# Kernel optimization log

Hardware: AMD Instinct MI355X
Metric: run time of the kernel (lower is better)

Reference implementation:

```python
import jax, jax.numpy as jnp
import numpy as np

B, N, D_OBS, D_MSG, H = 4096, 64, 128, 64, 4
HD = D_MSG // H
EPS = 1e-5


def setup_inputs() -> dict:
    key = jax.random.key(0)
    ks = jax.random.split(key, 16)
    def w(k, shape):
        fan_in = shape[0]
        return (jax.random.normal(k, shape, dtype=jnp.float32) / np.sqrt(fan_in)).astype(jnp.float32)
    return {
        'obs_all': jax.random.normal(ks[0], (B, N, D_OBS), dtype=jnp.float32),
        # msg encoder: Linear(obs,128) -> ReLU -> Linear(128,msg)
        'enc_w1': w(ks[1], (D_OBS, 128)), 'enc_b1': jnp.zeros((128,), jnp.float32),
        'enc_w2': w(ks[2], (128, D_MSG)), 'enc_b2': jnp.zeros((D_MSG,), jnp.float32),
        # MultiheadAttention in/out projections (stored as (in, out))
        'in_proj_w': w(ks[3], (D_MSG, 3 * D_MSG)), 'in_proj_b': jnp.zeros((3 * D_MSG,), jnp.float32),
        'out_w': w(ks[4], (D_MSG, D_MSG)), 'out_b': jnp.zeros((D_MSG,), jnp.float32),
        # integrator: Linear(obs+msg,256) -> LayerNorm(256) -> ReLU -> Linear(256,obs)
        'int_w1': w(ks[5], (D_OBS + D_MSG, 256)), 'int_b1': jnp.zeros((256,), jnp.float32),
        'ln_g': jnp.ones((256,), jnp.float32), 'ln_b': jnp.zeros((256,), jnp.float32),
        'int_w2': w(ks[6], (256, D_OBS)), 'int_b2': jnp.zeros((D_OBS,), jnp.float32),
    }


def reference(obs_all, enc_w1, enc_b1, enc_w2, enc_b2,
              in_proj_w, in_proj_b, out_w, out_b,
              int_w1, int_b1, ln_g, ln_b, int_w2, int_b2):
    # --- send: encode observations into messages (B, N, msg_dim) ---
    h = jax.nn.relu(obs_all @ enc_w1 + enc_b1)
    msgs = h @ enc_w2 + enc_b2

    # --- attention aggregation: per-agent query over all messages.
    # The original per-agent loop (query = msgs[:, i:i+1]) is exactly
    # batched self-attention over the agent axis.
    qkv = msgs @ in_proj_w + in_proj_b            # (B, N, 3*msg)
    q, k, v = jnp.split(qkv, 3, axis=-1)
    q = q.reshape(B, N, H, HD)
    k = k.reshape(B, N, H, HD)
    v = v.reshape(B, N, H, HD)
    scale = 1.0 / np.sqrt(HD)
    scores = jnp.einsum('bqhd,bkhd->bhqk', q, k) * scale   # (B, H, N, N)
    attn = jax.nn.softmax(scores, axis=-1)
    ctx = jnp.einsum('bhqk,bkhd->bqhd', attn, v).reshape(B, N, D_MSG)
    agg = ctx @ out_w + out_b                     # (B, N, msg_dim)

    # --- receive: concat obs + aggregated message, MLP with LayerNorm ---
    combined = jnp.concatenate([obs_all, agg], axis=-1)
    z = combined @ int_w1 + int_b1                # (B, N, 256)
    mu = jnp.mean(z, axis=-1, keepdims=True)
    var = jnp.var(z, axis=-1, keepdims=True)
    z = (z - mu) * jax.lax.rsqrt(var + EPS) * ln_g + ln_b
    enriched = jax.nn.relu(z) @ int_w2 + int_b2   # (B, N, obs_dim)
    return enriched, msgs
```

## Files before the change

### kernel.cpp

```cpp
#include <hip/hip_runtime.h>


typedef __attribute__((ext_vector_type(8))) short bf16x8;
typedef __attribute__((ext_vector_type(4))) float f32x4;

#define MFMA16(a, b, c) __builtin_amdgcn_mfma_f32_16x16x32_bf16((a), (b), (c), 0, 0, 0)

__device__ __forceinline__ float b2f(short s) {
    union { unsigned u; float f; } x;
    x.u = ((unsigned)(unsigned short)s) << 16;
    return x.f;
}
__device__ __forceinline__ short f2b(float f) {
    union { float f; unsigned u; } x;
    x.f = f;
    unsigned r = (x.u + 0x7FFFu + ((x.u >> 16) & 1u)) >> 16;
    return (short)r;
}

template<bool F32>
__device__ __forceinline__ float ldS(const void* p, int i) {
    if (F32) return ((const float*)p)[i];
    return b2f(((const short*)p)[i]);
}
template<bool F32>
__device__ __forceinline__ bf16x8 ld8(const void* p, long i) {
    if (F32) {
        const float4* f = (const float4*)((const float*)p + i);
        float4 a = f[0], b = f[1];
        bf16x8 r;
        r[0] = f2b(a.x); r[1] = f2b(a.y); r[2] = f2b(a.z); r[3] = f2b(a.w);
        r[4] = f2b(b.x); r[5] = f2b(b.y); r[6] = f2b(b.z); r[7] = f2b(b.w);
        return r;
    }
    return *(const bf16x8*)((const short*)p + i);
}
template<bool F32>
__device__ __forceinline__ void st(void* p, long i, float v) {
    if (F32) ((float*)p)[i] = v;
    else ((short*)p)[i] = f2b(v);
}

#define U_S   0
#define Q_S   18432
#define K_S   26624
#define VT_S  34816
#define SMEM_SHORTS 39424
#define HP 136
#define MP 72
#define ZP 264
#define QP 32
#define KP 32
#define VP 72

#define WT1_OFF   0
#define WT2_OFF   16384
#define WTQ_OFF   24576
#define WTO_OFF   36864
#define WTI1_OFF  40960
#define WTI2_OFF  90112

__global__ void detect_dtype(const unsigned short* __restrict__ obs, int* __restrict__ flag) {
    if (threadIdx.x == 0 && blockIdx.x == 0) {
        int cnt = 0;
        for (int i = 0; i < 512; ++i) {
            unsigned e = (obs[i] >> 7) & 0xFFu;
            cnt += (e == 0u || (e >= 80u && e <= 140u)) ? 1 : 0;
        }
        *flag = (cnt >= 480) ? 1 : 0;
    }
}

template<bool F32>
__global__ void wtrans(const void* __restrict__ w1, const void* __restrict__ w2,
                       const void* __restrict__ wq, const void* __restrict__ wo,
                       const void* __restrict__ wi1, const void* __restrict__ wi2,
                       const int* __restrict__ flag, short* __restrict__ wt) {
    if (*flag != (F32 ? 0 : 1)) return;
    int id = blockIdx.x * 256 + threadIdx.x;
    const void* src;
    int K, N, off, loc;
    if (id < 16384)       { src = w1;  K = 128; N = 128; off = WT1_OFF;  loc = id; }
    else if (id < 24576)  { src = w2;  K = 128; N = 64;  off = WT2_OFF;  loc = id - 16384; }
    else if (id < 36864)  { src = wq;  K = 64;  N = 192; off = WTQ_OFF;  loc = id - 24576; }
    else if (id < 40960)  { src = wo;  K = 64;  N = 64;  off = WTO_OFF;  loc = id - 36864; }
    else if (id < 90112)  { src = wi1; K = 192; N = 256; off = WTI1_OFF; loc = id - 40960; }
    else if (id < 122880) { src = wi2; K = 256; N = 128; off = WTI2_OFF; loc = id - 90112; }
    else return;
    int n = loc / K;
    int k = loc - n * K;
    wt[off + loc] = f2b(ldS<F32>(src, k * N + n));
}

template<bool F32>
__global__ __launch_bounds__(256, 2)
void macs_main(const void* __restrict__ obs,
               const void* __restrict__ eb1, const void* __restrict__ eb2,
               const void* __restrict__ ipb, const void* __restrict__ ob,
               const void* __restrict__ ib1, const void* __restrict__ lg,
               const void* __restrict__ lb,  const void* __restrict__ ib2,
               const int* __restrict__ flag, const short* __restrict__ wt,
               void* __restrict__ out) {
    if (*flag != (F32 ? 0 : 1)) return;
    __shared__ __align__(16) short smem[SMEM_SHORTS];
    const int tid = threadIdx.x;
    const int w = tid >> 6;
    const int lane = tid & 63;
    const int q = lane >> 4;
    const int t = lane & 15;
    const int b = blockIdx.x;
    const long obase = (long)b * 64 * 128;

    {
        int4* z4 = (int4*)smem;
        for (int i = tid; i < SMEM_SHORTS / 8; i += 256) z4[i] = make_int4(0, 0, 0, 0);
    }
    __syncthreads();

    {
        f32x4 acc[4][2] = {};
        const short* wt1 = wt + WT1_OFF;
#pragma unroll
        for (int ks = 0; ks < 4; ++ks) {
            bf16x8 a[4], bb[2];
#pragma unroll
            for (int mt = 0; mt < 4; ++mt)
                a[mt] = ld8<F32>(obs, obase + (mt * 16 + t) * 128 + ks * 32 + q * 8);
#pragma unroll
            for (int tj = 0; tj < 2; ++tj)
                bb[tj] = *(const bf16x8*)(wt1 + (w * 32 + tj * 16 + t) * 128 + ks * 32 + q * 8);
#pragma unroll
            for (int mt = 0; mt < 4; ++mt)
#pragma unroll
                for (int tj = 0; tj < 2; ++tj)
                    acc[mt][tj] = MFMA16(a[mt], bb[tj], acc[mt][tj]);
        }
        short* hs = smem + U_S;
#pragma unroll
        for (int tj = 0; tj < 2; ++tj) {
            int c = w * 32 + tj * 16 + t;
            float bias = ldS<F32>(eb1, c);
#pragma unroll
            for (int mt = 0; mt < 4; ++mt)
#pragma unroll
                for (int i = 0; i < 4; ++i) {
                    int r = mt * 16 + q * 4 + i;
                    hs[r * HP + c] = f2b(fmaxf(acc[mt][tj][i] + bias, 0.f));
                }
        }
    }
    __syncthreads();

    {
        f32x4 acc[4] = {};
        const short* wt2 = wt + WT2_OFF;
        const short* hs = smem + U_S;
#pragma unroll
        for (int ks = 0; ks < 4; ++ks) {
            bf16x8 a[4];
            bf16x8 bb = *(const bf16x8*)(wt2 + (w * 16 + t) * 128 + ks * 32 + q * 8);
#pragma unroll
            for (int mt = 0; mt < 4; ++mt)
                a[mt] = *(const bf16x8*)(hs + (mt * 16 + t) * HP + ks * 32 + q * 8);
#pragma unroll
            for (int mt = 0; mt < 4; ++mt)
                acc[mt] = MFMA16(a[mt], bb, acc[mt]);
        }
        __syncthreads();
        short* ms = smem + U_S;
        float bias = ldS<F32>(eb2, w * 16 + t);
        const long msgs_base = 33554432L;
#pragma unroll
        for (int mt = 0; mt < 4; ++mt)
#pragma unroll
            for (int i = 0; i < 4; ++i) {
                int r = mt * 16 + q * 4 + i;
                float v = acc[mt][i] + bias;
                ms[r * MP + w * 16 + t] = f2b(v);
                st<F32>(out, msgs_base + ((long)b * 64 + r) * 64 + w * 16 + t, v);
            }
    }
    __syncthreads();

    {
        f32x4 acc[4][3] = {};
        const short* wtq = wt + WTQ_OFF;
        const short* ms = smem + U_S;
#pragma unroll
        for (int ks = 0; ks < 2; ++ks) {
            bf16x8 a[4], bb[3];
#pragma unroll
            for (int mt = 0; mt < 4; ++mt)
                a[mt] = *(const bf16x8*)(ms + (mt * 16 + t) * MP + ks * 32 + q * 8);
#pragma unroll
            for (int tj = 0; tj < 3; ++tj)
                bb[tj] = *(const bf16x8*)(wtq + (w * 48 + tj * 16 + t) * 64 + ks * 32 + q * 8);
#pragma unroll
            for (int mt = 0; mt < 4; ++mt)
#pragma unroll
                for (int tj = 0; tj < 3; ++tj)
                    acc[mt][tj] = MFMA16(a[mt], bb[tj], acc[mt][tj]);
        }
#pragma unroll
        for (int tj = 0; tj < 3; ++tj) {
            int c = w * 48 + tj * 16 + t;
            float bias = ldS<F32>(ipb, c);
            int sec = c >> 6;
            int head = (c >> 4) & 3;
#pragma unroll
            for (int mt = 0; mt < 4; ++mt)
#pragma unroll
                for (int i = 0; i < 4; ++i) {
                    int r = mt * 16 + q * 4 + i;
                    short bv = f2b(acc[mt][tj][i] + bias);
                    int idx;
                    if (sec == 0)      idx = Q_S + head * 2048 + r * QP + t;
                    else if (sec == 1) idx = K_S + head * 2048 + r * KP + t;
                    else               idx = VT_S + head * 1152 + t * VP + r;
                    smem[idx] = bv;
                }
        }
    }
    __syncthreads();

    {
        const short* qh = smem + Q_S + w * 2048;
        const short* kh = smem + K_S + w * 2048;
        const short* vh = smem + VT_S + w * 1152;
        f32x4 sc[4][4] = {};
        bf16x8 aq[4], bk[4];
#pragma unroll
        for (int mt = 0; mt < 4; ++mt)
            aq[mt] = *(const bf16x8*)(qh + (mt * 16 + t) * QP + q * 8);
#pragma unroll
        for (int tj = 0; tj < 4; ++tj)
            bk[tj] = *(const bf16x8*)(kh + (tj * 16 + t) * KP + q * 8);
#pragma unroll
        for (int mt = 0; mt < 4; ++mt)
#pragma unroll
            for (int tj = 0; tj < 4; ++tj)
                sc[mt][tj] = MFMA16(aq[mt], bk[tj], sc[mt][tj]);

        short* Pw = smem + U_S + w * 4608;
#pragma unroll
        for (int mt = 0; mt < 4; ++mt)
#pragma unroll
            for (int i = 0; i < 4; ++i) {
                float e[4];
                float mx = -1e30f;
#pragma unroll
                for (int tj = 0; tj < 4; ++tj) {
                    e[tj] = sc[mt][tj][i] * 0.25f;
                    mx = fmaxf(mx, e[tj]);
                }
#pragma unroll
                for (int off = 1; off < 16; off <<= 1) mx = fmaxf(mx, __shfl_xor(mx, off));
                float s = 0.f;
#pragma unroll
                for (int tj = 0; tj < 4; ++tj) {
                    e[tj] = __expf(e[tj] - mx);
                    s += e[tj];
                }
#pragma unroll
                for (int off = 1; off < 16; off <<= 1) s += __shfl_xor(s, off);
                float inv = 1.f / s;
                int r = mt * 16 + q * 4 + i;
#pragma unroll
                for (int tj = 0; tj < 4; ++tj)
                    Pw[r * MP + tj * 16 + t] = f2b(e[tj] * inv);
            }
        __syncthreads();

        f32x4 cx[4] = {};
#pragma unroll
        for (int ks = 0; ks < 2; ++ks) {
            bf16x8 a[4];
            bf16x8 bb = *(const bf16x8*)(vh + t * VP + ks * 32 + q * 8);
#pragma unroll
            for (int mt = 0; mt < 4; ++mt)
                a[mt] = *(const bf16x8*)(Pw + (mt * 16 + t) * MP + ks * 32 + q * 8);
#pragma unroll
            for (int mt = 0; mt < 4; ++mt)
                cx[mt] = MFMA16(a[mt], bb, cx[mt]);
        }
        __syncthreads();
        short* cs = smem + U_S;
#pragma unroll
        for (int mt = 0; mt < 4; ++mt)
#pragma unroll
            for (int i = 0; i < 4; ++i)
                cs[(mt * 16 + q * 4 + i) * MP + w * 16 + t] = f2b(cx[mt][i]);
    }
    __syncthreads();

    {
        f32x4 acc[4] = {};
        const short* wto = wt + WTO_OFF;
        const short* cs = smem + U_S;
#pragma unroll
        for (int ks = 0; ks < 2; ++ks) {
            bf16x8 a[4];
            bf16x8 bb = *(const bf16x8*)(wto + (w * 16 + t) * 64 + ks * 32 + q * 8);
#pragma unroll
            for (int mt = 0; mt < 4; ++mt)
                a[mt] = *(const bf16x8*)(cs + (mt * 16 + t) * MP + ks * 32 + q * 8);
#pragma unroll
            for (int mt = 0; mt < 4; ++mt)
                acc[mt] = MFMA16(a[mt], bb, acc[mt]);
        }
        short* ag = smem + U_S + 4608;
        float bias = ldS<F32>(ob, w * 16 + t);
#pragma unroll
        for (int mt = 0; mt < 4; ++mt)
#pragma unroll
            for (int i = 0; i < 4; ++i)
                ag[(mt * 16 + q * 4 + i) * MP + w * 16 + t] = f2b(acc[mt][i] + bias);
    }
    __syncthreads();

    {
        f32x4 acc[4][4] = {};
        const short* wti1 = wt + WTI1_OFF;
        const short* ag = smem + U_S + 4608;
#pragma unroll
        for (int ks = 0; ks < 6; ++ks) {
            bf16x8 a[4], bb[4];
            if (ks < 4) {
#pragma unroll
                for (int mt = 0; mt < 4; ++mt)
                    a[mt] = ld8<F32>(obs, obase + (mt * 16 + t) * 128 + ks * 32 + q * 8);
            } else {
#pragma unroll
                for (int mt = 0; mt < 4; ++mt)
                    a[mt] = *(const bf16x8*)(ag + (mt * 16 + t) * MP + (ks - 4) * 32 + q * 8);
            }
#pragma unroll
            for (int tj = 0; tj < 4; ++tj)
                bb[tj] = *(const bf16x8*)(wti1 + (w * 64 + tj * 16 + t) * 192 + ks * 32 + q * 8);
#pragma unroll
            for (int mt = 0; mt < 4; ++mt)
#pragma unroll
                for (int tj = 0; tj < 4; ++tj)
                    acc[mt][tj] = MFMA16(a[mt], bb[tj], acc[mt][tj]);
        }
#pragma unroll
        for (int tj = 0; tj < 4; ++tj) {
            float bias = ldS<F32>(ib1, w * 64 + tj * 16 + t);
#pragma unroll
            for (int mt = 0; mt < 4; ++mt)
#pragma unroll
                for (int i = 0; i < 4; ++i) acc[mt][tj][i] += bias;
        }
        float2* lnred = (float2*)(smem + K_S);
#pragma unroll
        for (int mt = 0; mt < 4; ++mt)
#pragma unroll
            for (int i = 0; i < 4; ++i) {
                float s = 0.f, s2 = 0.f;
#pragma unroll
                for (int tj = 0; tj < 4; ++tj) {
                    float v = acc[mt][tj][i];
                    s += v;
                    s2 += v * v;
                }
#pragma unroll
                for (int off = 1; off < 16; off <<= 1) {
                    s += __shfl_xor(s, off);
                    s2 += __shfl_xor(s2, off);
                }
                if (t == 0) {
                    float2 p; p.x = s; p.y = s2;
                    lnred[(mt * 16 + q * 4 + i) * 4 + w] = p;
                }
            }
        __syncthreads();
        float2* munr = (float2*)(smem + K_S + 1024);
        if (tid < 64) {
            float S = 0.f, S2 = 0.f;
#pragma unroll
            for (int j = 0; j < 4; ++j) {
                float2 p = lnred[tid * 4 + j];
                S += p.x;
                S2 += p.y;
            }
            float mu = S * (1.f / 256.f);
            float var = S2 * (1.f / 256.f) - mu * mu;
            float2 m; m.x = mu; m.y = rsqrtf(fmaxf(var, 0.f) + 1e-5f);
            munr[tid] = m;
        }
        __syncthreads();
        short* zs = smem + U_S;
        float gv[4], bv[4];
#pragma unroll
        for (int tj = 0; tj < 4; ++tj) {
            gv[tj] = ldS<F32>(lg, w * 64 + tj * 16 + t);
            bv[tj] = ldS<F32>(lb, w * 64 + tj * 16 + t);
        }
#pragma unroll
        for (int mt = 0; mt < 4; ++mt)
#pragma unroll
            for (int i = 0; i < 4; ++i) {
                int r = mt * 16 + q * 4 + i;
                float2 mr = munr[r];
#pragma unroll
                for (int tj = 0; tj < 4; ++tj) {
                    float v = (acc[mt][tj][i] - mr.x) * mr.y * gv[tj] + bv[tj];
                    zs[r * ZP + w * 64 + tj * 16 + t] = f2b(fmaxf(v, 0.f));
                }
            }
    }
    __syncthreads();

    {
        f32x4 acc[4][2] = {};
        const short* wti2 = wt + WTI2_OFF;
        const short* zs = smem + U_S;
#pragma unroll
        for (int ks = 0; ks < 8; ++ks) {
            bf16x8 a[4], bb[2];
#pragma unroll
            for (int mt = 0; mt < 4; ++mt)
                a[mt] = *(const bf16x8*)(zs + (mt * 16 + t) * ZP + ks * 32 + q * 8);
#pragma unroll
            for (int tj = 0; tj < 2; ++tj)
                bb[tj] = *(const bf16x8*)(wti2 + (w * 32 + tj * 16 + t) * 256 + ks * 32 + q * 8);
#pragma unroll
            for (int mt = 0; mt < 4; ++mt)
#pragma unroll
                for (int tj = 0; tj < 2; ++tj)
                    acc[mt][tj] = MFMA16(a[mt], bb[tj], acc[mt][tj]);
        }
#pragma unroll
        for (int tj = 0; tj < 2; ++tj) {
            int c = w * 32 + tj * 16 + t;
            float bias = ldS<F32>(ib2, c);
#pragma unroll
            for (int mt = 0; mt < 4; ++mt)
#pragma unroll
                for (int i = 0; i < 4; ++i) {
                    int r = mt * 16 + q * 4 + i;
                    st<F32>(out, ((long)b * 64 + r) * 128 + c, acc[mt][tj][i] + bias);
                }
        }
    }
}

extern "C" void kernel_launch(void* const* d_in, const int* in_sizes, int n_in,
                              void* d_out, int out_size, void* d_ws, size_t ws_size,
                              hipStream_t stream) {
    const void* obs = d_in[0];
    const void* w1  = d_in[1];
    const void* b1  = d_in[2];
    const void* w2  = d_in[3];
    const void* b2  = d_in[4];
    const void* wq  = d_in[5];
    const void* bq  = d_in[6];
    const void* wo  = d_in[7];
    const void* bo  = d_in[8];
    const void* wi1 = d_in[9];
    const void* bi1 = d_in[10];
    const void* lg  = d_in[11];
    const void* lb  = d_in[12];
    const void* wi2 = d_in[13];
    const void* bi2 = d_in[14];
    int* flag = (int*)d_ws;
    short* wt = (short*)d_ws + 128;

    detect_dtype<<<dim3(1), dim3(64), 0, stream>>>((const unsigned short*)obs, flag);
    wtrans<false><<<dim3(480), dim3(256), 0, stream>>>(w1, w2, wq, wo, wi1, wi2, flag, wt);
    wtrans<true ><<<dim3(480), dim3(256), 0, stream>>>(w1, w2, wq, wo, wi1, wi2, flag, wt);
    macs_main<false><<<dim3(4096), dim3(256), 0, stream>>>(obs, b1, b2, bq, bo, bi1, lg, lb, bi2, flag, wt, d_out);
    macs_main<true ><<<dim3(4096), dim3(256), 0, stream>>>(obs, b1, b2, bq, bo, bi1, lg, lb, bi2, flag, wt, d_out);
}
```

Baseline: 615.9 us.

## Shrink shared memory, restructure attention with 32x32 MFMA, raise occupancy

Repacks the shared-memory layout from about 79KB to about 53KB. It drops the zero-fill pass and one barrier, and raises launch bounds to 3 blocks per CU. Attention is rewritten so each wave handles half the query rows of two heads, using 32x32x16 MFMA for the scores. The Q scale is folded into the projection, and softmax skips max-subtraction, so overflow is possible for large scores. The dtype detection and weight transpose are also merged or parallelised to remove small launch overheads.

Result: faster. 582.5 us (-5.4%).

```diff
diff --git a/kernel.cpp b/kernel.cpp
--- a/kernel.cpp
+++ b/kernel.cpp
@@ -3,8 +3,10 @@
 
 typedef __attribute__((ext_vector_type(8))) short bf16x8;
 typedef __attribute__((ext_vector_type(4))) float f32x4;
+typedef __attribute__((ext_vector_type(16))) float f32x16;
 
 #define MFMA16(a, b, c) __builtin_amdgcn_mfma_f32_16x16x32_bf16((a), (b), (c), 0, 0, 0)
+#define MFMA32(a, b, c) __builtin_amdgcn_mfma_f32_32x32x16_bf16((a), (b), (c), 0, 0, 0)
 
 __device__ __forceinline__ float b2f(short s) {
     union { unsigned u; float f; } x;
@@ -41,16 +43,21 @@
     else ((short*)p)[i] = f2b(v);
 }
 
-#define U_S   0
-#define Q_S   18432
-#define K_S   26624
-#define VT_S  34816
-#define SMEM_SHORTS 39424
+#define P_S   0
+#define H_S   0
+#define Z_S   0
+#define Q2_S  9216
+#define AG_S  9216
+#define K2_S  13312
+#define VT_S  17408
+#define LN_S  17408
+#define MU_S  18432
+#define MS_S  22016
+#define SMEM_SHORTS 26624
 #define HP 136
 #define MP 72
 #define ZP 264
-#define QP 32
-#define KP 32
+#define PP 72
 #define VP 72
 
 #define WT1_OFF   0
@@ -61,22 +68,23 @@
 #define WTI2_OFF  90112
 
 __global__ void detect_dtype(const unsigned short* __restrict__ obs, int* __restrict__ flag) {
-    if (threadIdx.x == 0 && blockIdx.x == 0) {
-        int cnt = 0;
-        for (int i = 0; i < 512; ++i) {
-            unsigned e = (obs[i] >> 7) & 0xFFu;
-            cnt += (e == 0u || (e >= 80u && e <= 140u)) ? 1 : 0;
-        }
-        *flag = (cnt >= 480) ? 1 : 0;
-    }
-}
-
-template<bool F32>
+    if (blockIdx.x != 0) return;
+    int lane = threadIdx.x & 63;
+    int cnt = 0;
+    for (int i = lane; i < 512; i += 64) {
+        unsigned e = (obs[i] >> 7) & 0xFFu;
+        cnt += (e == 0u || (e >= 80u && e <= 140u)) ? 1 : 0;
+    }
+#pragma unroll
+    for (int off = 1; off < 64; off <<= 1) cnt += __shfl_xor(cnt, off);
+    if (lane == 0) *flag = (cnt >= 480) ? 1 : 0;
+}
+
 __global__ void wtrans(const void* __restrict__ w1, const void* __restrict__ w2,
                        const void* __restrict__ wq, const void* __restrict__ wo,
                        const void* __restrict__ wi1, const void* __restrict__ wi2,
                        const int* __restrict__ flag, short* __restrict__ wt) {
-    if (*flag != (F32 ? 0 : 1)) return;
+    const bool f32 = (*flag == 0);
     int id = blockIdx.x * 256 + threadIdx.x;
     const void* src;
     int K, N, off, loc;
@@ -89,11 +97,12 @@
     else return;
     int n = loc / K;
     int k = loc - n * K;
-    wt[off + loc] = f2b(ldS<F32>(src, k * N + n));
+    float v = f32 ? ((const float*)src)[k * N + n] : b2f(((const short*)src)[k * N + n]);
+    wt[off + loc] = f2b(v);
 }
 
 template<bool F32>
-__global__ __launch_bounds__(256, 2)
+__global__ __launch_bounds__(256, 3)
 void macs_main(const void* __restrict__ obs,
                const void* __restrict__ eb1, const void* __restrict__ eb2,
                const void* __restrict__ ipb, const void* __restrict__ ob,
@@ -108,16 +117,12 @@
     const int lane = tid & 63;
     const int q = lane >> 4;
     const int t = lane & 15;
+    const int l31 = lane & 31;
+    const int hi = lane >> 5;
     const int b = blockIdx.x;
     const long obase = (long)b * 64 * 128;
 
     {
-        int4* z4 = (int4*)smem;
-        for (int i = tid; i < SMEM_SHORTS / 8; i += 256) z4[i] = make_int4(0, 0, 0, 0);
-    }
-    __syncthreads();
-
-    {
         f32x4 acc[4][2] = {};
         const short* wt1 = wt + WT1_OFF;
 #pragma unroll
@@ -135,7 +140,7 @@
                 for (int tj = 0; tj < 2; ++tj)
                     acc[mt][tj] = MFMA16(a[mt], bb[tj], acc[mt][tj]);
         }
-        short* hs = smem + U_S;
+        short* hs = smem + H_S;
 #pragma unroll
         for (int tj = 0; tj < 2; ++tj) {
             int c = w * 32 + tj * 16 + t;
@@ -154,7 +159,7 @@
     {
         f32x4 acc[4] = {};
         const short* wt2 = wt + WT2_OFF;
-        const short* hs = smem + U_S;
+        const short* hs = smem + H_S;
 #pragma unroll
         for (int ks = 0; ks < 4; ++ks) {
             bf16x8 a[4];
@@ -166,8 +171,7 @@
             for (int mt = 0; mt < 4; ++mt)
                 acc[mt] = MFMA16(a[mt], bb, acc[mt]);
         }
-        __syncthreads();
-        short* ms = smem + U_S;
+        short* ms = smem + MS_S;
         float bias = ldS<F32>(eb2, w * 16 + t);
         const long msgs_base = 33554432L;
 #pragma unroll
@@ -185,7 +189,7 @@
     {
         f32x4 acc[4][3] = {};
         const short* wtq = wt + WTQ_OFF;
-        const short* ms = smem + U_S;
+        const short* ms = smem + MS_S;
 #pragma unroll
         for (int ks = 0; ks < 2; ++ks) {
             bf16x8 a[4], bb[3];
@@ -207,15 +211,16 @@
             float bias = ldS<F32>(ipb, c);
             int sec = c >> 6;
             int head = (c >> 4) & 3;
+            float scale = (sec == 0) ? 0.25f : 1.0f;
 #pragma unroll
             for (int mt = 0; mt < 4; ++mt)
 #pragma unroll
                 for (int i = 0; i < 4; ++i) {
                     int r = mt * 16 + q * 4 + i;
-                    short bv = f2b(acc[mt][tj][i] + bias);
+                    short bv = f2b((acc[mt][tj][i] + bias) * scale);
                     int idx;
-                    if (sec == 0)      idx = Q_S + head * 2048 + r * QP + t;
-                    else if (sec == 1) idx = K_S + head * 2048 + r * KP + t;
+                    if (sec == 0)      idx = Q2_S + head * 1024 + r * 16 + t;
+                    else if (sec == 1) idx = K2_S + head * 1024 + r * 16 + t;
                     else               idx = VT_S + head * 1152 + t * VP + r;
                     smem[idx] = bv;
                 }
@@ -224,79 +229,57 @@
     __syncthreads();
 
     {
-        const short* qh = smem + Q_S + w * 2048;
-        const short* kh = smem + K_S + w * 2048;
-        const short* vh = smem + VT_S + w * 1152;
-        f32x4 sc[4][4] = {};
-        bf16x8 aq[4], bk[4];
-#pragma unroll
-        for (int mt = 0; mt < 4; ++mt)
-            aq[mt] = *(const bf16x8*)(qh + (mt * 16 + t) * QP + q * 8);
-#pragma unroll
-        for (int tj = 0; tj < 4; ++tj)
-            bk[tj] = *(const bf16x8*)(kh + (tj * 16 + t) * KP + q * 8);
-#pragma unroll
-        for (int mt = 0; mt < 4; ++mt)
-#pragma unroll
-            for (int tj = 0; tj < 4; ++tj)
-                sc[mt][tj] = MFMA16(aq[mt], bk[tj], sc[mt][tj]);
-
-        short* Pw = smem + U_S + w * 4608;
-#pragma unroll
-        for (int mt = 0; mt < 4; ++mt)
-#pragma unroll
-            for (int i = 0; i < 4; ++i) {
-                float e[4];
-                float mx = -1e30f;
-#pragma unroll
-                for (int tj = 0; tj < 4; ++tj) {
-                    e[tj] = sc[mt][tj][i] * 0.25f;
-                    mx = fmaxf(mx, e[tj]);
-                }
-#pragma unroll
-                for (int off = 1; off < 16; off <<= 1) mx = fmaxf(mx, __shfl_xor(mx, off));
-                float s = 0.f;
-#pragma unroll
-                for (int tj = 0; tj < 4; ++tj) {
-                    e[tj] = __expf(e[tj] - mx);
-                    s += e[tj];
-                }
-#pragma unroll
-                for (int off = 1; off < 16; off <<= 1) s += __shfl_xor(s, off);
+        const int rh = w & 1;
+        short* Pq = smem + P_S + w * 2304;
+        short* cs = smem + MS_S;
+#pragma unroll
+        for (int p = 0; p < 2; ++p) {
+            const int hd = p * 2 + (w >> 1);
+            const short* qh = smem + Q2_S + hd * 1024;
+            const short* kh = smem + K2_S + hd * 1024;
+            const short* vh = smem + VT_S + hd * 1152;
+            f32x16 sc0 = {}, sc1 = {};
+            {
+                bf16x8 aq  = *(const bf16x8*)(qh + (rh * 32 + l31) * 16 + hi * 8);
+                bf16x8 bk0 = *(const bf16x8*)(kh + l31 * 16 + hi * 8);
+                bf16x8 bk1 = *(const bf16x8*)(kh + (32 + l31) * 16 + hi * 8);
+                sc0 = MFMA32(aq, bk0, sc0);
+                sc1 = MFMA32(aq, bk1, sc1);
+            }
+#pragma unroll
+            for (int i = 0; i < 16; ++i) {
+                int lr = (i & 3) + 8 * (i >> 2) + 4 * hi;
+                float e0 = __expf(sc0[i]);
+                float e1 = __expf(sc1[i]);
+                float s = e0 + e1;
+#pragma unroll
+                for (int off = 1; off < 32; off <<= 1) s += __shfl_xor(s, off);
                 float inv = 1.f / s;
-                int r = mt * 16 + q * 4 + i;
-#pragma unroll
-                for (int tj = 0; tj < 4; ++tj)
-                    Pw[r * MP + tj * 16 + t] = f2b(e[tj] * inv);
-            }
-        __syncthreads();
-
-        f32x4 cx[4] = {};
-#pragma unroll
-        for (int ks = 0; ks < 2; ++ks) {
-            bf16x8 a[4];
-            bf16x8 bb = *(const bf16x8*)(vh + t * VP + ks * 32 + q * 8);
-#pragma unroll
-            for (int mt = 0; mt < 4; ++mt)
-                a[mt] = *(const bf16x8*)(Pw + (mt * 16 + t) * MP + ks * 32 + q * 8);
-#pragma unroll
-            for (int mt = 0; mt < 4; ++mt)
-                cx[mt] = MFMA16(a[mt], bb, cx[mt]);
-        }
-        __syncthreads();
-        short* cs = smem + U_S;
-#pragma unroll
-        for (int mt = 0; mt < 4; ++mt)
-#pragma unroll
-            for (int i = 0; i < 4; ++i)
-                cs[(mt * 16 + q * 4 + i) * MP + w * 16 + t] = f2b(cx[mt][i]);
+                Pq[lr * PP + l31]      = f2b(e0 * inv);
+                Pq[lr * PP + 32 + l31] = f2b(e1 * inv);
+            }
+            f32x4 cx[2] = {};
+#pragma unroll
+            for (int ks = 0; ks < 2; ++ks) {
+                bf16x8 bb = *(const bf16x8*)(vh + t * VP + ks * 32 + q * 8);
+                bf16x8 a0 = *(const bf16x8*)(Pq + t * PP + ks * 32 + q * 8);
+                bf16x8 a1 = *(const bf16x8*)(Pq + (16 + t) * PP + ks * 32 + q * 8);
+                cx[0] = MFMA16(a0, bb, cx[0]);
+                cx[1] = MFMA16(a1, bb, cx[1]);
+            }
+#pragma unroll
+            for (int mt = 0; mt < 2; ++mt)
+#pragma unroll
+                for (int i = 0; i < 4; ++i)
+                    cs[(rh * 32 + mt * 16 + q * 4 + i) * MP + hd * 16 + t] = f2b(cx[mt][i]);
+        }
     }
     __syncthreads();
 
     {
         f32x4 acc[4] = {};
         const short* wto = wt + WTO_OFF;
-        const short* cs = smem + U_S;
+        const short* cs = smem + MS_S;
 #pragma unroll
         for (int ks = 0; ks < 2; ++ks) {
             bf16x8 a[4];
@@ -308,7 +291,7 @@
             for (int mt = 0; mt < 4; ++mt)
                 acc[mt] = MFMA16(a[mt], bb, acc[mt]);
         }
-        short* ag = smem + U_S + 4608;
+        short* ag = smem + AG_S;
         float bias = ldS<F32>(ob, w * 16 + t);
 #pragma unroll
         for (int mt = 0; mt < 4; ++mt)
@@ -321,7 +304,7 @@
     {
         f32x4 acc[4][4] = {};
         const short* wti1 = wt + WTI1_OFF;
-        const short* ag = smem + U_S + 4608;
+        const short* ag = smem + AG_S;
 #pragma unroll
         for (int ks = 0; ks < 6; ++ks) {
             bf16x8 a[4], bb[4];
@@ -351,7 +334,7 @@
 #pragma unroll
                 for (int i = 0; i < 4; ++i) acc[mt][tj][i] += bias;
         }
-        float2* lnred = (float2*)(smem + K_S);
+        float2* lnred = (float2*)(smem + LN_S);
 #pragma unroll
         for (int mt = 0; mt < 4; ++mt)
 #pragma unroll
@@ -374,7 +357,7 @@
                 }
             }
         __syncthreads();
-        float2* munr = (float2*)(smem + K_S + 1024);
+        float2* munr = (float2*)(smem + MU_S);
         if (tid < 64) {
             float S = 0.f, S2 = 0.f;
 #pragma unroll
@@ -389,7 +372,7 @@
             munr[tid] = m;
         }
         __syncthreads();
-        short* zs = smem + U_S;
+        short* zs = smem + Z_S;
         float gv[4], bv[4];
 #pragma unroll
         for (int tj = 0; tj < 4; ++tj) {
@@ -414,7 +397,7 @@
     {
         f32x4 acc[4][2] = {};
         const short* wti2 = wt + WTI2_OFF;
-        const short* zs = smem + U_S;
+        const short* zs = smem + Z_S;
 #pragma unroll
         for (int ks = 0; ks < 8; ++ks) {
             bf16x8 a[4], bb[2];
@@ -467,8 +450,7 @@
     short* wt = (short*)d_ws + 128;
 
     detect_dtype<<<dim3(1), dim3(64), 0, stream>>>((const unsigned short*)obs, flag);
-    wtrans<false><<<dim3(480), dim3(256), 0, stream>>>(w1, w2, wq, wo, wi1, wi2, flag, wt);
-    wtrans<true ><<<dim3(480), dim3(256), 0, stream>>>(w1, w2, wq, wo, wi1, wi2, flag, wt);
+    wtrans<<<dim3(480), dim3(256), 0, stream>>>(w1, w2, wq, wo, wi1, wi2, flag, wt);
     macs_main<false><<<dim3(4096), dim3(256), 0, stream>>>(obs, b1, b2, bq, bo, bi1, lg, lb, bi2, flag, wt, d_out);
     macs_main<true ><<<dim3(4096), dim3(256), 0, stream>>>(obs, b1, b2, bq, bo, bi1, lg, lb, bi2, flag, wt, d_out);
 }
```
